# Kernel tuning notes

Hardware: AMD Instinct MI355X
Metric: run time of the kernel (lower is better)

Reference implementation:

```python
import jax, jax.numpy as jnp
import numpy as np


def setup_inputs() -> dict:
    key = jax.random.key(0)
    k1, k2 = jax.random.split(key)
    B, N, M, D = 4, 8192, 8192, 3
    inp = jax.random.normal(k1, (B, N, D), dtype=jnp.float32)
    pnt = jax.random.normal(k2, (B, M, D), dtype=jnp.float32)
    return {"input": inp, "point": pnt}


def reference(input, point):
    # Per-query nearest-neighbor squared distance:
    # out[b, n] = min_m || input[b, n] - point[b, m] ||^2
    # Use ||a||^2 + ||b||^2 - 2 a.b to avoid materializing [B, N, M, D].
    sq_in = jnp.sum(input * input, axis=-1)          # [B, N]
    sq_pt = jnp.sum(point * point, axis=-1)          # [B, M]
    cross = jnp.einsum('bnd,bmd->bnm', input, point) # [B, N, M]
    d2 = sq_in[:, :, None] + sq_pt[:, None, :] - 2.0 * cross
    d2 = jnp.maximum(d2, 0.0)  # numerical guard
    return jnp.min(d2, axis=-1)  # [B, N]
```

## Files before the change

kernel.cpp:

```cpp
#include <hip/hip_runtime.h>
#include <hip/hip_bf16.h>

constexpr int B = 4;
constexpr int N = 8192;
constexpr int M = 8192;

constexpr int QPW     = 64;
constexpr int WAVES   = 4;
constexpr int QB      = QPW * WAVES;
constexpr int QTILES  = N / QB;
constexpr int PCHUNKS = 16;
constexpr int CHUNK   = M / PCHUNKS;
constexpr int PTILES  = CHUNK / 32;

typedef __bf16 bf16x8 __attribute__((ext_vector_type(8)));
typedef float  f32x16 __attribute__((ext_vector_type(16)));

union FragU { uint4 u; bf16x8 b; };

__device__ __host__ inline unsigned f2bf(float x) {
    unsigned u = __float_as_uint(x);
    return (u + 0x7FFFu + ((u >> 16) & 1u)) >> 16;
}
__device__ inline float bf2f(unsigned b) { return __uint_as_float(b << 16); }
__device__ inline unsigned pk(unsigned lo, unsigned hi) { return lo | (hi << 16); }


__global__ __launch_bounds__(256) void prep_kernel(const float* __restrict__ point,
                                                   uint4* __restrict__ wtab,
                                                   unsigned int* __restrict__ out) {
    int i = blockIdx.x * 256 + threadIdx.x;
    if (i >= B * M) return;
    const float p0 = point[3 * i + 0];
    const float p1 = point[3 * i + 1];
    const float p2 = point[3 * i + 2];
    const float v0 = -2.0f * p0, v1 = -2.0f * p1, v2 = -2.0f * p2;
    const unsigned h0 = f2bf(v0), l0 = f2bf(v0 - bf2f(h0));
    const unsigned h1 = f2bf(v1), l1 = f2bf(v1 - bf2f(h1));
    const unsigned h2 = f2bf(v2), l2 = f2bf(v2 - bf2f(h2));
    const float s = fmaf(p0, p0, fmaf(p1, p1, p2 * p2));
    const unsigned sh = f2bf(s), sl = f2bf(s - bf2f(sh));
    uint4 f0, f1;
    f0.x = pk(h0, h0); f0.y = pk(l0, l0); f0.z = pk(h1, h1); f0.w = pk(l1, l1);
    f1.x = pk(h2, h2); f1.y = pk(l2, l2); f1.z = pk(sh, sl); f1.w = 0;
    wtab[2 * i + 0] = f0;
    wtab[2 * i + 1] = f1;
    out[i] = 0x7F7F7F7Fu;
}

__device__ inline FragU make_bfrag(const float* __restrict__ input,
                                   int b, int q, int h, float& sq_a) {
    const float* a = input + ((size_t)b * N + q) * 3;
    const float a0 = a[0], a1 = a[1], a2 = a[2];
    sq_a = fmaf(a0, a0, fmaf(a1, a1, a2 * a2));
    const unsigned ah0 = f2bf(a0), al0 = f2bf(a0 - bf2f(ah0));
    const unsigned ah1 = f2bf(a1), al1 = f2bf(a1 - bf2f(ah1));
    const unsigned ah2 = f2bf(a2), al2 = f2bf(a2 - bf2f(ah2));
    FragU bq;
    const unsigned dA = h ? pk(ah2, al2) : pk(ah0, al0);
    const unsigned dB = h ? 0x3F803F80u  : pk(ah1, al1);
    bq.u.x = dA;
    bq.u.y = dA;
    bq.u.z = dB;
    bq.u.w = h ? 0u : dB;
    return bq;
}

__global__ __launch_bounds__(256, 3) void main_kernel(const float* __restrict__ input,
                                                      const uint4* __restrict__ wtab,
                                                      unsigned int* __restrict__ out) {
    const int bid    = blockIdx.x;
    const int pchunk = bid % PCHUNKS;
    const int qtile  = (bid / PCHUNKS) % QTILES;
    const int b      = bid / (PCHUNKS * QTILES);
    const int tid    = threadIdx.x;
    const int wave   = tid >> 6;
    const int lane   = tid & 63;
    const int col    = lane & 31;
    const int h      = lane >> 5;

    const int q0 = qtile * QB + wave * QPW + col;
    const int q1 = q0 + 32;
    float sq_a0, sq_a1;
    const FragU b0 = make_bfrag(input, b, q0, h, sq_a0);
    const FragU b1 = make_bfrag(input, b, q1, h, sq_a1);

    const uint4* __restrict__ wp =
        wtab + ((size_t)b * M + (size_t)pchunk * CHUNK) * 2;

    f32x16 cz, rmin0, rmin1;
#pragma unroll
    for (int i = 0; i < 16; ++i) { cz[i] = 0.0f; rmin0[i] = 1e30f; rmin1[i] = 1e30f; }

    for (int t = 0; t < PTILES; t += 2) {
        FragU fa0, fa1;
        fa0.u = wp[((t * 32 + col) << 1) + h];
        fa1.u = wp[(((t + 1) * 32 + col) << 1) + h];
        f32x16 acc00 = __builtin_amdgcn_mfma_f32_32x32x16_bf16(fa0.b, b0.b, cz, 0, 0, 0);
        f32x16 acc01 = __builtin_amdgcn_mfma_f32_32x32x16_bf16(fa0.b, b1.b, cz, 0, 0, 0);
        f32x16 acc10 = __builtin_amdgcn_mfma_f32_32x32x16_bf16(fa1.b, b0.b, cz, 0, 0, 0);
        f32x16 acc11 = __builtin_amdgcn_mfma_f32_32x32x16_bf16(fa1.b, b1.b, cz, 0, 0, 0);
#pragma unroll
        for (int i = 0; i < 16; ++i) {
            rmin0[i] = fminf(rmin0[i], fminf(acc00[i], acc10[i]));
            rmin1[i] = fminf(rmin1[i], fminf(acc01[i], acc11[i]));
        }
    }

    float m0 = rmin0[0], m1 = rmin1[0];
#pragma unroll
    for (int i = 1; i < 16; ++i) { m0 = fminf(m0, rmin0[i]); m1 = fminf(m1, rmin1[i]); }
    m0 = fminf(m0, __shfl_xor(m0, 32, 64));
    m1 = fminf(m1, __shfl_xor(m1, 32, 64));

    if (lane < 32) {
        atomicMin(&out[(size_t)b * N + q0], __float_as_uint(fmaxf(m0 + sq_a0, 0.0f)));
        atomicMin(&out[(size_t)b * N + q1], __float_as_uint(fmaxf(m1 + sq_a1, 0.0f)));
    }
}

extern "C" void kernel_launch(void* const* d_in, const int* in_sizes, int n_in,
                              void* d_out, int out_size, void* d_ws, size_t ws_size,
                              hipStream_t stream) {
    const float* input = (const float*)d_in[0];
    const float* point = (const float*)d_in[1];
    unsigned int* out  = (unsigned int*)d_out;

    uint4* wtab = (uint4*)d_ws;

    const int prep_grid = (B * M + 255) / 256;
    const int main_grid = B * QTILES * PCHUNKS;

    prep_kernel<<<prep_grid, 256, 0, stream>>>(point, wtab, out);
    main_kernel<<<main_grid, 256, 0, stream>>>(input, wtab, out);
}
```

Measured before the change: 66.32 us.

## Fuse point preprocessing into main kernel and replace atomics with LDS reduction

```diff
diff --git a/kernel.cpp b/kernel.cpp
--- a/kernel.cpp
+++ b/kernel.cpp
@@ -1,64 +1,45 @@
 #include <hip/hip_runtime.h>
-#include <hip/hip_bf16.h>
 
 constexpr int B = 4;
 constexpr int N = 8192;
 constexpr int M = 8192;
 
-constexpr int QPW     = 64;
-constexpr int WAVES   = 4;
-constexpr int QB      = QPW * WAVES;
-constexpr int QTILES  = N / QB;
-constexpr int PCHUNKS = 16;
-constexpr int CHUNK   = M / PCHUNKS;
-constexpr int PTILES  = CHUNK / 32;
+constexpr int QB     = 64;
+constexpr int WAVES  = 4;
+constexpr int QTILES = N / QB;
+constexpr int MPW    = M / WAVES;
+constexpr int TILES  = MPW / 32;
 
 typedef __bf16 bf16x8 __attribute__((ext_vector_type(8)));
 typedef float  f32x16 __attribute__((ext_vector_type(16)));
 
 union FragU { uint4 u; bf16x8 b; };
 
-__device__ __host__ inline unsigned f2bf(float x) {
-    unsigned u = __float_as_uint(x);
-    return (u + 0x7FFFu + ((u >> 16) & 1u)) >> 16;
-}
-__device__ inline float bf2f(unsigned b) { return __uint_as_float(b << 16); }
-__device__ inline unsigned pk(unsigned lo, unsigned hi) { return lo | (hi << 16); }
 
-
-__global__ __launch_bounds__(256) void prep_kernel(const float* __restrict__ point,
-                                                   uint4* __restrict__ wtab,
-                                                   unsigned int* __restrict__ out) {
-    int i = blockIdx.x * 256 + threadIdx.x;
-    if (i >= B * M) return;
-    const float p0 = point[3 * i + 0];
-    const float p1 = point[3 * i + 1];
-    const float p2 = point[3 * i + 2];
-    const float v0 = -2.0f * p0, v1 = -2.0f * p1, v2 = -2.0f * p2;
-    const unsigned h0 = f2bf(v0), l0 = f2bf(v0 - bf2f(h0));
-    const unsigned h1 = f2bf(v1), l1 = f2bf(v1 - bf2f(h1));
-    const unsigned h2 = f2bf(v2), l2 = f2bf(v2 - bf2f(h2));
-    const float s = fmaf(p0, p0, fmaf(p1, p1, p2 * p2));
-    const unsigned sh = f2bf(s), sl = f2bf(s - bf2f(sh));
-    uint4 f0, f1;
-    f0.x = pk(h0, h0); f0.y = pk(l0, l0); f0.z = pk(h1, h1); f0.w = pk(l1, l1);
-    f1.x = pk(h2, h2); f1.y = pk(l2, l2); f1.z = pk(sh, sl); f1.w = 0;
-    wtab[2 * i + 0] = f0;
-    wtab[2 * i + 1] = f1;
-    out[i] = 0x7F7F7F7Fu;
+__device__ inline void split_rep(float v, unsigned& hh, unsigned& ll) {
+    const unsigned u = __float_as_uint(v);
+    const unsigned t = u & 0xFFFF0000u;
+    hh = t | (t >> 16);
+    const unsigned r = __float_as_uint(v - __uint_as_float(t)) & 0xFFFF0000u;
+    ll = r | (r >> 16);
 }
 
-__device__ inline FragU make_bfrag(const float* __restrict__ input,
-                                   int b, int q, int h, float& sq_a) {
-    const float* a = input + ((size_t)b * N + q) * 3;
-    const float a0 = a[0], a1 = a[1], a2 = a[2];
+__device__ inline unsigned split_pair(float v) {
+    const unsigned u = __float_as_uint(v);
+    const unsigned t = u & 0xFFFF0000u;
+    const unsigned r = __float_as_uint(v - __uint_as_float(t)) & 0xFFFF0000u;
+    return (t >> 16) | r;
+}
+
+__device__ inline FragU make_bfrag(const float* __restrict__ a3, int h, float& sq_a) {
+    const float a0 = a3[0], a1 = a3[1], a2 = a3[2];
     sq_a = fmaf(a0, a0, fmaf(a1, a1, a2 * a2));
-    const unsigned ah0 = f2bf(a0), al0 = f2bf(a0 - bf2f(ah0));
-    const unsigned ah1 = f2bf(a1), al1 = f2bf(a1 - bf2f(ah1));
-    const unsigned ah2 = f2bf(a2), al2 = f2bf(a2 - bf2f(ah2));
+    const unsigned d0 = split_pair(a0);
+    const unsigned d1 = split_pair(a1);
+    const unsigned d2 = split_pair(a2);
     FragU bq;
-    const unsigned dA = h ? pk(ah2, al2) : pk(ah0, al0);
-    const unsigned dB = h ? 0x3F803F80u  : pk(ah1, al1);
+    const unsigned dA = h ? d2 : d0;
+    const unsigned dB = h ? 0x3F803F80u : d1;
     bq.u.x = dA;
     bq.u.y = dA;
     bq.u.z = dB;
@@ -66,36 +47,51 @@
     return bq;
 }
 
-__global__ __launch_bounds__(256, 3) void main_kernel(const float* __restrict__ input,
-                                                      const uint4* __restrict__ wtab,
-                                                      unsigned int* __restrict__ out) {
-    const int bid    = blockIdx.x;
-    const int pchunk = bid % PCHUNKS;
-    const int qtile  = (bid / PCHUNKS) % QTILES;
-    const int b      = bid / (PCHUNKS * QTILES);
-    const int tid    = threadIdx.x;
-    const int wave   = tid >> 6;
-    const int lane   = tid & 63;
-    const int col    = lane & 31;
-    const int h      = lane >> 5;
+__device__ inline FragU make_afrag(const float* __restrict__ p3, int h) {
+    const float p0 = p3[0], p1 = p3[1], p2 = p3[2];
+    const float s  = fmaf(p0, p0, fmaf(p1, p1, p2 * p2));
+    unsigned h0, l0, h1, l1, h2, l2;
+    split_rep(-2.0f * p0, h0, l0);
+    split_rep(-2.0f * p1, h1, l1);
+    split_rep(-2.0f * p2, h2, l2);
+    const unsigned us = __float_as_uint(s) & 0xFFFF0000u;
+    const unsigned rs = __float_as_uint(s - __uint_as_float(us)) & 0xFFFF0000u;
+    const unsigned shsl = (us >> 16) | rs;
+    FragU fa;
+    fa.u.x = h ? h2 : h0;
+    fa.u.y = h ? l2 : l0;
+    fa.u.z = h ? shsl : h1;
+    fa.u.w = h ? 0u : l1;
+    return fa;
+}
 
-    const int q0 = qtile * QB + wave * QPW + col;
+__global__ __launch_bounds__(256, 2) void nn_kernel(const float* __restrict__ input,
+                                                    const float* __restrict__ point,
+                                                    float* __restrict__ out) {
+    const int bid   = blockIdx.x;
+    const int qtile = bid % QTILES;
+    const int b     = bid / QTILES;
+    const int tid   = threadIdx.x;
+    const int wave  = tid >> 6;
+    const int lane  = tid & 63;
+    const int col   = lane & 31;
+    const int h     = lane >> 5;
+
+    const int q0 = qtile * QB + col;
     const int q1 = q0 + 32;
     float sq_a0, sq_a1;
-    const FragU b0 = make_bfrag(input, b, q0, h, sq_a0);
-    const FragU b1 = make_bfrag(input, b, q1, h, sq_a1);
+    const FragU b0 = make_bfrag(input + ((size_t)b * N + q0) * 3, h, sq_a0);
+    const FragU b1 = make_bfrag(input + ((size_t)b * N + q1) * 3, h, sq_a1);
 
-    const uint4* __restrict__ wp =
-        wtab + ((size_t)b * M + (size_t)pchunk * CHUNK) * 2;
+    const float* __restrict__ pbase = point + ((size_t)b * M + wave * MPW) * 3;
 
     f32x16 cz, rmin0, rmin1;
 #pragma unroll
     for (int i = 0; i < 16; ++i) { cz[i] = 0.0f; rmin0[i] = 1e30f; rmin1[i] = 1e30f; }
 
-    for (int t = 0; t < PTILES; t += 2) {
-        FragU fa0, fa1;
-        fa0.u = wp[((t * 32 + col) << 1) + h];
-        fa1.u = wp[(((t + 1) * 32 + col) << 1) + h];
+    for (int t = 0; t < TILES; t += 2) {
+        const FragU fa0 = make_afrag(pbase + 3 * (t * 32 + col), h);
+        const FragU fa1 = make_afrag(pbase + 3 * ((t + 1) * 32 + col), h);
         f32x16 acc00 = __builtin_amdgcn_mfma_f32_32x32x16_bf16(fa0.b, b0.b, cz, 0, 0, 0);
         f32x16 acc01 = __builtin_amdgcn_mfma_f32_32x32x16_bf16(fa0.b, b1.b, cz, 0, 0, 0);
         f32x16 acc10 = __builtin_amdgcn_mfma_f32_32x32x16_bf16(fa1.b, b0.b, cz, 0, 0, 0);
@@ -113,9 +109,17 @@
     m0 = fminf(m0, __shfl_xor(m0, 32, 64));
     m1 = fminf(m1, __shfl_xor(m1, 32, 64));
 
+    __shared__ float red[WAVES][QB];
     if (lane < 32) {
-        atomicMin(&out[(size_t)b * N + q0], __float_as_uint(fmaxf(m0 + sq_a0, 0.0f)));
-        atomicMin(&out[(size_t)b * N + q1], __float_as_uint(fmaxf(m1 + sq_a1, 0.0f)));
+        red[wave][col]      = m0;
+        red[wave][col + 32] = m1;
+    }
+    __syncthreads();
+    if (tid < QB) {
+        const float m = fminf(fminf(red[0][tid], red[1][tid]),
+                              fminf(red[2][tid], red[3][tid]));
+        const float sq = (tid < 32) ? sq_a0 : sq_a1;
+        out[(size_t)b * N + (size_t)qtile * QB + tid] = fmaxf(m + sq, 0.0f);
     }
 }
 
@@ -124,13 +128,9 @@
                               hipStream_t stream) {
     const float* input = (const float*)d_in[0];
     const float* point = (const float*)d_in[1];
-    unsigned int* out  = (unsigned int*)d_out;
+    float* out         = (float*)d_out;
 
-    uint4* wtab = (uint4*)d_ws;
+    (void)d_ws; (void)ws_size;
 
-    const int prep_grid = (B * M + 255) / 256;
-    const int main_grid = B * QTILES * PCHUNKS;
-
-    prep_kernel<<<prep_grid, 256, 0, stream>>>(point, wtab, out);
-    main_kernel<<<main_grid, 256, 0, stream>>>(input, wtab, out);
+    nn_kernel<<<B * QTILES, 256, 0, stream>>>(input, point, out);
 }
```

After: 71.97 us. +8.5%, slower.
